# Kernel tuning notes

Hardware: AMD Instinct MI355X
Metric: run time of the kernel (lower is better)

The kernel has to match this reference:

```python
import jax, jax.numpy as jnp
import numpy as np

B, C, H, W = 8, 256, 64, 64
C8 = C // 8


def setup_inputs() -> dict:
    key = jax.random.key(0)
    ks = jax.random.split(key, 8)
    scale = 0.05
    return {
        "x": jax.random.normal(ks[0], (B, C, H, W), jnp.float32),
        "Wf": jax.random.normal(ks[1], (C8, C), jnp.float32) * scale,
        "bf": jax.random.normal(ks[2], (C8,), jnp.float32) * scale,
        "Wg": jax.random.normal(ks[3], (C8, C), jnp.float32) * scale,
        "bg": jax.random.normal(ks[4], (C8,), jnp.float32) * scale,
        "Wh": jax.random.normal(ks[5], (C, C), jnp.float32) * scale,
        "bh": jax.random.normal(ks[6], (C,), jnp.float32) * scale,
        "gamma": jax.random.normal(ks[7], (1,), jnp.float32) * scale,
    }


def reference(x, Wf, bf, Wg, bg, Wh, bh, gamma):
    b, c, h, w = x.shape
    n = h * w
    xr = x.reshape(b, c, n)  # flatten spatial: [B, C, N]
    # 1x1 convs == per-pixel linear projections
    f = jnp.einsum('oc,bcn->bon', Wf, xr) + bf[None, :, None]  # [B, C/8, N]
    g = jnp.einsum('oc,bcn->bon', Wg, xr) + bg[None, :, None]  # [B, C/8, N]
    hh = jnp.einsum('oc,bcn->bon', Wh, xr) + bh[None, :, None]  # [B, C, N]
    # s = f^T @ g : unscaled attention logits, [B, N, N]
    s = jnp.einsum('bki,bkj->bij', f, g)
    attention = jax.nn.softmax(s, axis=-1)
    # out = h @ attention^T : out[b,c,i] = sum_j h[b,c,j] * attn[b,i,j]
    out = jnp.einsum('bcj,bij->bci', hh, attention)
    out = out.reshape(b, c, w, h)  # original code uses (W, H); H==W here
    out = gamma[0] * out + x
    return (out, attention)
```

## Files before the change

kernel.cpp:

```cpp
#include <hip/hip_runtime.h>
#include <hip/hip_bf16.h>

typedef unsigned short u16;
typedef __attribute__((ext_vector_type(8))) short short8;
typedef __attribute__((ext_vector_type(4))) float f32x4;

#define BATCH 8
#define CH 256
#define NPIX 4096
#define KD 32

static __device__ __forceinline__ u16 f2bf(float f) {
  union { __hip_bfloat16 h; u16 u; } cv;
  cv.h = __float2bfloat16(f);
  return cv.u;
}

static __device__ __forceinline__ float bf2f(u16 u) {
  union { unsigned int i; float f; } cv;
  cv.i = ((unsigned int)u) << 16;
  return cv.f;
}

__global__ __launch_bounds__(256) void proj_kernel(
    const float* __restrict__ x,
    const float* __restrict__ Wf, const float* __restrict__ bfp,
    const float* __restrict__ Wg, const float* __restrict__ bgp,
    const float* __restrict__ Wh, const float* __restrict__ bhp,
    u16* __restrict__ fT, u16* __restrict__ gT, u16* __restrict__ hhb)
{
  __shared__ float xs[CH][36];
  const int b  = blockIdx.x >> 7;
  const int n0 = (blockIdx.x & 127) * 32;
  const int t  = threadIdx.x;

  const float* xb = x + ((size_t)b * CH) * NPIX + n0;
  #pragma unroll
  for (int kk = 0; kk < 8; ++kk) {
    int v = kk * 256 + t;
    int c = v >> 3, p4 = v & 7;
    float4 d = *(const float4*)(xb + (size_t)c * NPIX + p4 * 4);
    *(float4*)&xs[c][p4 * 4] = d;
  }
  __syncthreads();

  const int o = t;
  float acch[32];
  #pragma unroll
  for (int p = 0; p < 32; ++p) acch[p] = bhp[o];

  const int o2 = t & 63;
  const int oo = o2 & 31;
  const bool isf = o2 < 32;
  const float* Wfg = isf ? Wf : Wg;
  const float bias2 = isf ? bfp[oo] : bgp[oo];
  const int pg = (t >> 6) * 8;
  float accf[8];
  #pragma unroll
  for (int p = 0; p < 8; ++p) accf[p] = bias2;

  const float* whr  = Wh  + o * CH;
  const float* wfgr = Wfg + oo * CH;
  for (int c = 0; c < CH; c += 4) {
    float4 wh4 = *(const float4*)(whr + c);
    float4 wf4 = *(const float4*)(wfgr + c);
    float wha[4] = {wh4.x, wh4.y, wh4.z, wh4.w};
    float wfa[4] = {wf4.x, wf4.y, wf4.z, wf4.w};
    #pragma unroll
    for (int cc = 0; cc < 4; ++cc) {
      float wh = wha[cc], wf = wfa[cc];
      #pragma unroll
      for (int p4 = 0; p4 < 8; ++p4) {
        float4 xv = *(const float4*)&xs[c + cc][p4 * 4];
        acch[p4*4+0] = fmaf(wh, xv.x, acch[p4*4+0]);
        acch[p4*4+1] = fmaf(wh, xv.y, acch[p4*4+1]);
        acch[p4*4+2] = fmaf(wh, xv.z, acch[p4*4+2]);
        acch[p4*4+3] = fmaf(wh, xv.w, acch[p4*4+3]);
      }
      #pragma unroll
      for (int p = 0; p < 8; ++p) accf[p] = fmaf(wf, xs[c + cc][pg + p], accf[p]);
    }
  }

  u16* hrow = hhb + ((size_t)b * CH + o) * NPIX + n0;
  #pragma unroll
  for (int q = 0; q < 4; ++q) {
    uint4 u;
    u.x = f2bf(acch[q*8+0]) | ((unsigned)f2bf(acch[q*8+1]) << 16);
    u.y = f2bf(acch[q*8+2]) | ((unsigned)f2bf(acch[q*8+3]) << 16);
    u.z = f2bf(acch[q*8+4]) | ((unsigned)f2bf(acch[q*8+5]) << 16);
    u.w = f2bf(acch[q*8+6]) | ((unsigned)f2bf(acch[q*8+7]) << 16);
    *(uint4*)(hrow + q * 8) = u;
  }
  u16* dst = (isf ? fT : gT) + ((size_t)b * NPIX + n0 + pg) * KD + oo;
  #pragma unroll
  for (int p = 0; p < 8; ++p) dst[(size_t)p * KD] = f2bf(accf[p]);
}

__global__ __launch_bounds__(512, 4) void fused_attn_pv(
    const u16* __restrict__ fT, const u16* __restrict__ gT,
    const u16* __restrict__ hhb, const float* __restrict__ x,
    const float* __restrict__ gamma,
    float* __restrict__ attn_out, float* __restrict__ outp)
{
  __shared__ u16 Pt[2][64 * 64];
  __shared__ float part[8][64];
  __shared__ float invs[64];

  const int bid = blockIdx.x;
  const int b  = bid & 7;
  const int n0 = (bid >> 3) * 64;
  const int t  = threadIdx.x;
  const int iw = t >> 6, l = t & 63;
  const int lg = l >> 4, lm = l & 15;

  const u16* fb = fT + ((size_t)b * NPIX + n0) * KD;
  const u16* gb = gT + (size_t)b * NPIX * KD;
  const u16* hb = hhb + (size_t)b * CH * NPIX;

  f32x4 z4 = {0.f, 0.f, 0.f, 0.f};

  short8 ff[4];
  #pragma unroll
  for (int it = 0; it < 4; ++it)
    ff[it] = *(const short8*)(fb + (it * 16 + lm) * KD + lg * 8);

  float sum[4][4];
  #pragma unroll
  for (int it = 0; it < 4; ++it)
    #pragma unroll
    for (int r = 0; r < 4; ++r) sum[it][r] = 0.f;

  const int j1 = iw * 512;
  for (int jt = 0; jt < 32; ++jt) {
    int j0 = j1 + jt * 16;
    short8 gf = *(const short8*)(gb + (size_t)(j0 + lm) * KD + lg * 8);
    #pragma unroll
    for (int it = 0; it < 4; ++it) {
      f32x4 s = __builtin_amdgcn_mfma_f32_16x16x32_bf16(ff[it], gf, z4, 0, 0, 0);
      #pragma unroll
      for (int r = 0; r < 4; ++r) sum[it][r] += __expf(s[r]);
    }
  }
  #pragma unroll
  for (int m = 1; m < 16; m <<= 1)
    #pragma unroll
    for (int it = 0; it < 4; ++it)
      #pragma unroll
      for (int r = 0; r < 4; ++r) sum[it][r] += __shfl_xor(sum[it][r], m, 64);
  if (lm == 0) {
    #pragma unroll
    for (int it = 0; it < 4; ++it)
      #pragma unroll
      for (int r = 0; r < 4; ++r) part[iw][it * 16 + lg * 4 + r] = sum[it][r];
  }
  __syncthreads();
  if (t < 64) {
    float s = 0.f;
    #pragma unroll
    for (int w2 = 0; w2 < 8; ++w2) s += part[w2][t];
    invs[t] = 1.0f / s;
  }
  __syncthreads();

  const int it2 = iw >> 1, jsub = iw & 1;
  float inv4[4];
  #pragma unroll
  for (int r = 0; r < 4; ++r) inv4[r] = invs[it2 * 16 + lg * 4 + r];
  const short8 f2 = ff[it2];

  float* abase = attn_out + ((size_t)b * NPIX + n0) * NPIX;
  const int srow = t >> 3;
  const int scol = (t & 7) * 8;
  const int rdbyte = srow * 128 + ((scol * 2) ^ ((srow & 7) << 4));

  f32x4 acc[2][4];
  #pragma unroll
  for (int mf = 0; mf < 2; ++mf)
    #pragma unroll
    for (int nf = 0; nf < 4; ++nf) acc[mf][nf] = z4;

  short8 gP[2], gQ[2];

  auto LDG = [&](short8 (&g2)[2], int JC) {
    #pragma unroll
    for (int st = 0; st < 2; ++st)
      g2[st] = *(const short8*)(gb + (size_t)(JC + jsub * 32 + st * 16 + lm) * KD + lg * 8);
  };

  auto HALF = [&](u16* buf, short8 (&gc)[2], short8 (&gn)[2], int JC, int JN) {
    f32x4 s0 = __builtin_amdgcn_mfma_f32_16x16x32_bf16(f2, gc[0], z4, 0, 0, 0);
    f32x4 s1 = __builtin_amdgcn_mfma_f32_16x16x32_bf16(f2, gc[1], z4, 0, 0, 0);
    LDG(gn, JN);
    short8 hc[2][2];
    #pragma unroll
    for (int m = 0; m < 2; ++m)
      #pragma unroll
      for (int ks = 0; ks < 2; ++ks)
        hc[m][ks] = *(const short8*)(hb + (size_t)(iw * 32 + m * 16 + lm) * NPIX
                                     + JC + ks * 32 + lg * 8);
    const int ibyte = (it2 * 16 + lg * 4) * 128;
    #pragma unroll
    for (int r = 0; r < 4; ++r) {
      float p0 = __expf(s0[r]) * inv4[r];
      float p1 = __expf(s1[r]) * inv4[r];
      int row = ibyte + r * 128;
      int sw  = ((lg * 4 + r) & 7) << 4;
      int j0  = (jsub * 32 + lm) * 2;
      *(u16*)((char*)buf + row + (j0 ^ sw)) = f2bf(p0);
      *(u16*)((char*)buf + row + ((j0 + 32) ^ sw)) = f2bf(p1);
    }
    asm volatile("s_waitcnt lgkmcnt(0)\n\ts_barrier" ::: "memory");
    __builtin_amdgcn_s_setprio(1);
    #pragma unroll
    for (int nf = 0; nf < 4; ++nf) {
      #pragma unroll
      for (int ks = 0; ks < 2; ++ks) {
        int byte = (nf * 16 + lm) * 128 + (((ks * 4 + lg) * 16) ^ ((lm & 7) << 4));
        short8 pfr = *(const short8*)((char*)buf + byte);
        acc[0][nf] = __builtin_amdgcn_mfma_f32_16x16x32_bf16(hc[0][ks], pfr, acc[0][nf], 0, 0, 0);
        acc[1][nf] = __builtin_amdgcn_mfma_f32_16x16x32_bf16(hc[1][ks], pfr, acc[1][nf], 0, 0, 0);
      }
    }
    __builtin_amdgcn_s_setprio(0);
    short8 pw = *(const short8*)((char*)buf + rdbyte);
    f32x4 o0, o1;
    #pragma unroll
    for (int q = 0; q < 4; ++q) { o0[q] = bf2f((u16)pw[q]); o1[q] = bf2f((u16)pw[q + 4]); }
    float* dst = abase + (size_t)srow * NPIX + JC + scol;
    __builtin_nontemporal_store(o0, (f32x4*)dst);
    __builtin_nontemporal_store(o1, (f32x4*)(dst + 4));
  };

  LDG(gP, 0);
  for (int jc = 0; jc < NPIX; jc += 128) {
    int n1 = (jc + 64) & (NPIX - 1);
    int n2 = (jc + 128) & (NPIX - 1);
    HALF(&Pt[0][0], gP, gQ, jc, n1);
    HALF(&Pt[1][0], gQ, gP, jc + 64, n2);
  }

  const float gm = gamma[0];
  #pragma unroll
  for (int mf = 0; mf < 2; ++mf) {
    #pragma unroll
    for (int r = 0; r < 4; ++r) {
      int c = iw * 32 + mf * 16 + lg * 4 + r;
      #pragma unroll
      for (int nf = 0; nf < 4; ++nf) {
        int i = n0 + nf * 16 + lm;
        size_t idx = ((size_t)b * CH + c) * NPIX + i;
        outp[idx] = fmaf(gm, acc[mf][nf][r], x[idx]);
      }
    }
  }
}

extern "C" void kernel_launch(void* const* d_in, const int* in_sizes, int n_in,
                              void* d_out, int out_size, void* d_ws, size_t ws_size,
                              hipStream_t stream) {
  const float* x     = (const float*)d_in[0];
  const float* Wf    = (const float*)d_in[1];
  const float* bf    = (const float*)d_in[2];
  const float* Wg    = (const float*)d_in[3];
  const float* bg    = (const float*)d_in[4];
  const float* Wh    = (const float*)d_in[5];
  const float* bh    = (const float*)d_in[6];
  const float* gamma = (const float*)d_in[7];

  float* outp = (float*)d_out;
  float* attn_out = outp + (size_t)BATCH * CH * NPIX;

  u16* fT = (u16*)d_ws;
  u16* gT = fT + (size_t)BATCH * NPIX * KD;
  u16* hh = gT + (size_t)BATCH * NPIX * KD;

  proj_kernel<<<dim3(BATCH * (NPIX / 32)), dim3(256), 0, stream>>>(
      x, Wf, bf, Wg, bg, Wh, bh, fT, gT, hh);

  fused_attn_pv<<<dim3(BATCH * (NPIX / 64)), dim3(512), 0, stream>>>(
      fT, gT, hh, x, gamma, attn_out, outp);
}
```

Before: 360.0 us.

## Widen attention chunk to 128 columns and overlap P store with PV MFMAs

```diff
diff --git a/kernel.cpp b/kernel.cpp
--- a/kernel.cpp
+++ b/kernel.cpp
@@ -103,7 +103,7 @@
     const float* __restrict__ gamma,
     float* __restrict__ attn_out, float* __restrict__ outp)
 {
-  __shared__ u16 Pt[2][64 * 64];
+  __shared__ u16 Pt[2][64 * 128];
   __shared__ float part[8][64];
   __shared__ float invs[64];
 
@@ -171,8 +171,9 @@
 
   float* abase = attn_out + ((size_t)b * NPIX + n0) * NPIX;
   const int srow = t >> 3;
-  const int scol = (t & 7) * 8;
-  const int rdbyte = srow * 128 + ((scol * 2) ^ ((srow & 7) << 4));
+  const int sc   = (t & 7) * 16;
+  const int rb0 = srow * 256 + ((sc * 2) ^ ((srow & 7) << 4));
+  const int rb1 = srow * 256 + (((sc + 8) * 2) ^ ((srow & 7) << 4));
 
   f32x4 acc[2][4];
   #pragma unroll
@@ -180,64 +181,93 @@
     #pragma unroll
     for (int nf = 0; nf < 4; ++nf) acc[mf][nf] = z4;
 
-  short8 gP[2], gQ[2];
-
-  auto LDG = [&](short8 (&g2)[2], int JC) {
-    #pragma unroll
-    for (int st = 0; st < 2; ++st)
-      g2[st] = *(const short8*)(gb + (size_t)(JC + jsub * 32 + st * 16 + lm) * KD + lg * 8);
+  short8 gP[4], gQ[4];
+
+  auto LDG = [&](short8 (&g4)[4], int JC) {
+    #pragma unroll
+    for (int st = 0; st < 4; ++st)
+      g4[st] = *(const short8*)(gb + (size_t)(JC + jsub * 64 + st * 16 + lm) * KD + lg * 8);
   };
 
-  auto HALF = [&](u16* buf, short8 (&gc)[2], short8 (&gn)[2], int JC, int JN) {
-    f32x4 s0 = __builtin_amdgcn_mfma_f32_16x16x32_bf16(f2, gc[0], z4, 0, 0, 0);
-    f32x4 s1 = __builtin_amdgcn_mfma_f32_16x16x32_bf16(f2, gc[1], z4, 0, 0, 0);
-    LDG(gn, JN);
-    short8 hc[2][2];
-    #pragma unroll
-    for (int m = 0; m < 2; ++m)
-      #pragma unroll
-      for (int ks = 0; ks < 2; ++ks)
-        hc[m][ks] = *(const short8*)(hb + (size_t)(iw * 32 + m * 16 + lm) * NPIX
-                                     + JC + ks * 32 + lg * 8);
-    const int ibyte = (it2 * 16 + lg * 4) * 128;
-    #pragma unroll
-    for (int r = 0; r < 4; ++r) {
-      float p0 = __expf(s0[r]) * inv4[r];
-      float p1 = __expf(s1[r]) * inv4[r];
-      int row = ibyte + r * 128;
-      int sw  = ((lg * 4 + r) & 7) << 4;
-      int j0  = (jsub * 32 + lm) * 2;
-      *(u16*)((char*)buf + row + (j0 ^ sw)) = f2bf(p0);
-      *(u16*)((char*)buf + row + ((j0 + 32) ^ sw)) = f2bf(p1);
-    }
+  const u16* hrow0 = hb + (size_t)(iw * 32 + lm) * NPIX + lg * 8;
+  const u16* hrow1 = hb + (size_t)(iw * 32 + 16 + lm) * NPIX + lg * 8;
+
+  auto CHUNK = [&](u16* buf, short8 (&gc)[4], short8 (&gn)[4], int JC, int JN) {
+    #pragma unroll
+    for (int half = 0; half < 2; ++half) {
+      f32x4 sA = __builtin_amdgcn_mfma_f32_16x16x32_bf16(f2, gc[half*2+0], z4, 0, 0, 0);
+      f32x4 sB = __builtin_amdgcn_mfma_f32_16x16x32_bf16(f2, gc[half*2+1], z4, 0, 0, 0);
+      if (half == 0) LDG(gn, JN);
+      const int ibyte = (it2 * 16 + lg * 4) * 256;
+      #pragma unroll
+      for (int r = 0; r < 4; ++r) {
+        float pA = __expf(sA[r]) * inv4[r];
+        float pB = __expf(sB[r]) * inv4[r];
+        int row = ibyte + r * 256;
+        int sw  = ((lg * 4 + r) & 7) << 4;
+        int jA  = (jsub * 64 + half * 32 + lm) * 2;
+        *(u16*)((char*)buf + row + (jA ^ sw)) = f2bf(pA);
+        *(u16*)((char*)buf + row + ((jA + 32) ^ sw)) = f2bf(pB);
+      }
+    }
+    short8 hA00 = *(const short8*)(hrow0 + JC);
+    short8 hA10 = *(const short8*)(hrow1 + JC);
+    short8 hA01 = *(const short8*)(hrow0 + JC + 32);
+    short8 hA11 = *(const short8*)(hrow1 + JC + 32);
     asm volatile("s_waitcnt lgkmcnt(0)\n\ts_barrier" ::: "memory");
+    short8 hB00 = *(const short8*)(hrow0 + JC + 64);
+    short8 hB10 = *(const short8*)(hrow1 + JC + 64);
+    short8 hB01 = *(const short8*)(hrow0 + JC + 96);
+    short8 hB11 = *(const short8*)(hrow1 + JC + 96);
+    {
+      short8 pw0 = *(const short8*)((char*)buf + rb0);
+      short8 pw1 = *(const short8*)((char*)buf + rb1);
+      f32x4 o0, o1, o2, o3;
+      #pragma unroll
+      for (int q = 0; q < 4; ++q) {
+        o0[q] = bf2f((u16)pw0[q]);     o1[q] = bf2f((u16)pw0[q + 4]);
+        o2[q] = bf2f((u16)pw1[q]);     o3[q] = bf2f((u16)pw1[q + 4]);
+      }
+      float* dst = abase + (size_t)srow * NPIX + JC + sc;
+      __builtin_nontemporal_store(o0, (f32x4*)dst);
+      __builtin_nontemporal_store(o1, (f32x4*)(dst + 4));
+      __builtin_nontemporal_store(o2, (f32x4*)(dst + 8));
+      __builtin_nontemporal_store(o3, (f32x4*)(dst + 12));
+    }
     __builtin_amdgcn_s_setprio(1);
     #pragma unroll
-    for (int nf = 0; nf < 4; ++nf) {
-      #pragma unroll
-      for (int ks = 0; ks < 2; ++ks) {
-        int byte = (nf * 16 + lm) * 128 + (((ks * 4 + lg) * 16) ^ ((lm & 7) << 4));
+    for (int ks = 0; ks < 2; ++ks) {
+      #pragma unroll
+      for (int nf = 0; nf < 4; ++nf) {
+        int byte = (nf * 16 + lm) * 256 + (((ks * 64) + lg * 16) ^ ((lm & 7) << 4));
         short8 pfr = *(const short8*)((char*)buf + byte);
-        acc[0][nf] = __builtin_amdgcn_mfma_f32_16x16x32_bf16(hc[0][ks], pfr, acc[0][nf], 0, 0, 0);
-        acc[1][nf] = __builtin_amdgcn_mfma_f32_16x16x32_bf16(hc[1][ks], pfr, acc[1][nf], 0, 0, 0);
+        acc[0][nf] = __builtin_amdgcn_mfma_f32_16x16x32_bf16(
+            ks == 0 ? hA00 : hA01, pfr, acc[0][nf], 0, 0, 0);
+        acc[1][nf] = __builtin_amdgcn_mfma_f32_16x16x32_bf16(
+            ks == 0 ? hA10 : hA11, pfr, acc[1][nf], 0, 0, 0);
+      }
+    }
+    #pragma unroll
+    for (int ks = 0; ks < 2; ++ks) {
+      #pragma unroll
+      for (int nf = 0; nf < 4; ++nf) {
+        int byte = (nf * 16 + lm) * 256 + (((128 + ks * 64) + lg * 16) ^ ((lm & 7) << 4));
+        short8 pfr = *(const short8*)((char*)buf + byte);
+        acc[0][nf] = __builtin_amdgcn_mfma_f32_16x16x32_bf16(
+            ks == 0 ? hB00 : hB01, pfr, acc[0][nf], 0, 0, 0);
+        acc[1][nf] = __builtin_amdgcn_mfma_f32_16x16x32_bf16(
+            ks == 0 ? hB10 : hB11, pfr, acc[1][nf], 0, 0, 0);
       }
     }
     __builtin_amdgcn_s_setprio(0);
-    short8 pw = *(const short8*)((char*)buf + rdbyte);
-    f32x4 o0, o1;
-    #pragma unroll
-    for (int q = 0; q < 4; ++q) { o0[q] = bf2f((u16)pw[q]); o1[q] = bf2f((u16)pw[q + 4]); }
-    float* dst = abase + (size_t)srow * NPIX + JC + scol;
-    __builtin_nontemporal_store(o0, (f32x4*)dst);
-    __builtin_nontemporal_store(o1, (f32x4*)(dst + 4));
   };
 
   LDG(gP, 0);
-  for (int jc = 0; jc < NPIX; jc += 128) {
-    int n1 = (jc + 64) & (NPIX - 1);
-    int n2 = (jc + 128) & (NPIX - 1);
-    HALF(&Pt[0][0], gP, gQ, jc, n1);
-    HALF(&Pt[1][0], gQ, gP, jc + 64, n2);
+  for (int jc = 0; jc < NPIX; jc += 256) {
+    int n1 = (jc + 128) & (NPIX - 1);
+    int n2 = (jc + 256) & (NPIX - 1);
+    CHUNK(&Pt[0][0], gP, gQ, jc, n1);
+    CHUNK(&Pt[1][0], gQ, gP, jc + 128, n2);
   }
 
   const float gm = gamma[0];
```

Result: slower. 710.7 us (+97.4%).
